# Performance work log

Measured on AMD Instinct MI355X. Metric: run time of the kernel, lower is better.

The kernel has to match this reference:

```python
import jax, jax.numpy as jnp
import numpy as np

HIDDEN = 768
HEADS = 12
ORDERS = 3
NEG = -1e9


def setup_inputs() -> dict:
    key = jax.random.key(0)
    ks = jax.random.split(key, 16)
    B, N = 8, 512
    s = 0.02
    inp = {
        "v": jax.random.normal(ks[0], (B, N, HIDDEN), jnp.float32),
        "k": jax.random.normal(ks[1], (B, N, HIDDEN), jnp.float32),
        "q": jax.random.normal(ks[2], (B, N, HIDDEN), jnp.float32),
        "masks": jax.random.bernoulli(ks[3], 0.1, (ORDERS, B, 1, N, N)),
        "tau": 1,
        "training": 0,
        "Wv": jax.random.normal(ks[4], (HIDDEN, HIDDEN), jnp.float32) * s,
        "bv": jnp.zeros((HIDDEN,), jnp.float32),
        "Wk": jax.random.normal(ks[5], (HIDDEN, HIDDEN), jnp.float32) * s,
        "bk": jnp.zeros((HIDDEN,), jnp.float32),
        "Wq": jax.random.normal(ks[6], (HIDDEN, HIDDEN), jnp.float32) * s,
        "bq": jnp.zeros((HIDDEN,), jnp.float32),
        "Wm": jax.random.normal(ks[7], (HIDDEN, HIDDEN), jnp.float32) * s,
        "bm": jnp.zeros((HIDDEN,), jnp.float32),
        "pool_w": jax.random.normal(ks[8], (HIDDEN, 1), jnp.float32) * s,
        "pool_b": jnp.zeros((1,), jnp.float32),
        "mlp_w1": jax.random.normal(ks[9], (HIDDEN, HIDDEN // 2), jnp.float32) * s,
        "mlp_w2": jax.random.normal(ks[10], (HIDDEN // 2, ORDERS), jnp.float32) * s,
        "mlp_b2": jnp.zeros((ORDERS,), jnp.float32),
    }
    return inp


def _soft_routing(x, pool_w, pool_b, mlp_w1, mlp_w2, mlp_b2):
    # pooling='fc': masked attention pooling over sequence, then 2-layer MLP + softmax
    pad = (jnp.sum(jnp.abs(x), axis=-1) == 0)[:, :, None]        # [B, N, 1]
    scores = x @ pool_w + pool_b                                  # [B, N, 1]
    scores = jnp.where(pad, NEG, scores)
    scores = jax.nn.softmax(scores, axis=1)
    pooled = jnp.sum(x * scores, axis=1)                          # [B, HIDDEN]
    logits = jax.nn.relu(pooled @ mlp_w1) @ mlp_w2 + mlp_b2       # [B, L]
    return jax.nn.softmax(logits, axis=-1)


def reference(v, k, q, masks, tau, training, Wv, bv, Wk, bk, Wq, bq, Wm, bm,
              pool_w, pool_b, mlp_w1, mlp_w2, mlp_b2):
    B, N, _ = q.shape
    dk = HIDDEN // HEADS
    alphas = _soft_routing(v, pool_w, pool_b, mlp_w1, mlp_w2, mlp_b2)  # [B, L]

    def split_heads(x):
        return x.reshape(B, N, HEADS, dk).transpose(0, 2, 1, 3)  # [B, H, N, dk]

    vh = split_heads(v @ Wv + bv)
    kh = split_heads(k @ Wk + bk)
    qh = split_heads(q @ Wq + bq)

    scores = jnp.einsum('bhnd,bhmd->bhnm', qh, kh) / jnp.sqrt(jnp.float32(dk))
    # masks: [L, B, 1, N, N] broadcast over heads -> att_list [L, B, H, N, N]
    masked = jnp.where(masks[:, :, :, :, :], NEG, scores[None])
    att_list = jax.nn.softmax(masked, axis=-1)                    # [L, B, H, N, N]
    att_map = jnp.einsum('bl,lbhnm->bhnm', alphas, att_list)
    atted = jnp.einsum('bhnm,bhmd->bhnd', att_map, vh)
    atted = atted.transpose(0, 2, 1, 3).reshape(B, N, HIDDEN)
    return atted @ Wm + bm
```

## Files before the change

### kernel.cpp

```cpp
#include <hip/hip_runtime.h>
#include <hip/hip_bf16.h>
#include <stdint.h>


typedef __bf16 bf16x8 __attribute__((ext_vector_type(8)));
typedef float f32x4 __attribute__((ext_vector_type(4)));

#define NEGV -1e9f
#define SBFE(x, off) (((int)((x) << (31 - (off)))) >> 31)

__device__ __forceinline__ float b2f(unsigned short h) {
    union { unsigned int u; float f; } x; x.u = ((unsigned int)h) << 16; return x.f;
}
__device__ __forceinline__ unsigned short f2b(float f) {
    union { float f; unsigned int u; } x; x.f = f;
    unsigned int u = x.u + 0x7FFFu + ((x.u >> 16) & 1u);
    return (unsigned short)(u >> 16);
}
__device__ __forceinline__ unsigned int packbf(unsigned int u0, unsigned int u1) {
    unsigned int r0 = (u0 + 0x7FFFu + ((u0 >> 16) & 1u)) >> 16;
    unsigned int r1 = (u1 + 0x7FFFu + ((u1 >> 16) & 1u)) & 0xFFFF0000u;
    return r0 | r1;
}
__device__ __forceinline__ uint4 load8bf(const void* base, size_t elemOff, int isF32) {
    if (!isF32) return *(const uint4*)((const unsigned short*)base + elemOff);
    const uint4* f = (const uint4*)((const float*)base + elemOff);
    uint4 a = f[0], b = f[1];
    uint4 r;
    r.x = packbf(a.x, a.y);
    r.y = packbf(a.z, a.w);
    r.z = packbf(b.x, b.y);
    r.w = packbf(b.z, b.w);
    return r;
}
__device__ __forceinline__ float loadF(const void* p, int idx, int isF32) {
    return isF32 ? ((const float*)p)[idx] : b2f(((const unsigned short*)p)[idx]);
}

__global__ void sniff_kernel(const unsigned int* __restrict__ mp,
                             const unsigned int* __restrict__ vp,
                             const unsigned int* __restrict__ wp,
                             int* __restrict__ flags)
{
    __shared__ int oki, oku, okf, badv, badw;
    if (threadIdx.x == 0) { oki = 1; oku = 1; okf = 1; badv = 0; badw = 0; }
    __syncthreads();
    int li = 1, lu = 1, lf = 1, bv = 0, bw = 0;
    const uint4* m4 = (const uint4*)mp;
    for (int i = threadIdx.x; i < 4096; i += 256) {
        uint4 u = m4[i];
        unsigned int ws[4] = {u.x, u.y, u.z, u.w};
        #pragma unroll
        for (int j = 0; j < 4; j++) {
            unsigned int w = ws[j];
            if (w > 1u) li = 0;
            if (w & 0xFEFEFEFEu) lu = 0;
            if (w != 0u && w != 0x3F800000u) lf = 0;
        }
    }
    const uint4* v4 = (const uint4*)vp;
    const uint4* w4 = (const uint4*)wp;
    for (int i = threadIdx.x; i < 2048; i += 256) {
        uint4 u = v4[i];
        uint4 u2 = w4[i];
        unsigned int wa[4] = {u.x, u.y, u.z, u.w};
        unsigned int wb[4] = {u2.x, u2.y, u2.z, u2.w};
        #pragma unroll
        for (int j = 0; j < 4; j++) {
            float f0 = b2f((unsigned short)(wa[j] & 0xFFFF));
            float f1 = b2f((unsigned short)(wa[j] >> 16));
            if (!(fabsf(f0) < 1e4f) || !(fabsf(f1) < 1e4f)) bv = 1;
            f0 = b2f((unsigned short)(wb[j] & 0xFFFF));
            f1 = b2f((unsigned short)(wb[j] >> 16));
            if (!(fabsf(f0) < 1e4f) || !(fabsf(f1) < 1e4f)) bw = 1;
        }
    }
    if (!li) atomicAnd(&oki, 0);
    if (!lu) atomicAnd(&oku, 0);
    if (!lf) atomicAnd(&okf, 0);
    if (bv) atomicOr(&badv, 1);
    if (bw) atomicOr(&badw, 1);
    __syncthreads();
    if (threadIdx.x == 0) {
        flags[0] = oki ? 0 : (oku ? 1 : (okf ? 2 : 3));
        flags[1] = badv;
        flags[2] = badw;
    }
}

__global__ __launch_bounds__(256) void conv_act_kernel(
        const void* __restrict__ v, const void* __restrict__ k,
        const void* __restrict__ q, const int* __restrict__ flags,
        unsigned short* __restrict__ vb, unsigned short* __restrict__ kb,
        unsigned short* __restrict__ qb)
{
    const int dtV = flags[1];
    const int which = blockIdx.y;
    const void* src = (which == 0) ? v : (which == 1) ? k : q;
    unsigned short* dst = (which == 0) ? vb : (which == 1) ? kb : qb;
    size_t off = ((size_t)blockIdx.x * 256 + threadIdx.x) * 8;
    uint4 r = load8bf(src, off, dtV);
    *(uint4*)(dst + off) = r;
}

__global__ __launch_bounds__(256) void conv_wt_kernel(
        const void* __restrict__ W0, const void* __restrict__ W1,
        const void* __restrict__ W2, const void* __restrict__ W3,
        const int* __restrict__ flags,
        unsigned short* __restrict__ T0, unsigned short* __restrict__ T1,
        unsigned short* __restrict__ T2, unsigned short* __restrict__ T3)
{
    __shared__ unsigned short tile[64][65];
    const int t = threadIdx.x;
    const int dtW = flags[2];
    const int which = blockIdx.y;
    const void* W = (which == 0) ? W0 : (which == 1) ? W1 : (which == 2) ? W2 : W3;
    unsigned short* T = (which == 0) ? T0 : (which == 1) ? T1 : (which == 2) ? T2 : T3;
    const int tk = (blockIdx.x / 12) << 6;
    const int tn = (blockIdx.x % 12) << 6;
    #pragma unroll
    for (int i = 0; i < 16; i++) {
        int idx = (i << 8) + t;
        int r = idx >> 6, c = idx & 63;
        tile[r][c] = f2b(loadF(W, (tk + r) * 768 + tn + c, dtW));
    }
    __syncthreads();
    #pragma unroll
    for (int i = 0; i < 16; i++) {
        int idx = (i << 8) + t;
        int rn = idx >> 6, ck = idx & 63;
        T[(size_t)(tn + rn) * 768 + tk + ck] = tile[ck][rn];
    }
}

__global__ __launch_bounds__(256) void pack_kernel(
        const void* __restrict__ masks, const int* __restrict__ flags,
        unsigned int* __restrict__ pm)
{
    __shared__ unsigned char flg[32 * 512];
    const int t = threadIdx.x;
    const int mode = flags[0];
    const size_t e0 = (size_t)blockIdx.x * (32 * 512);
    if (mode == 0 || mode == 2) {
        const uint4* p = (const uint4*)((const unsigned int*)masks + e0);
        for (int i = t; i < 4096; i += 256) {
            uint4 u = p[i];
            int base = i << 2;
            flg[base + 0] = u.x ? 1 : 0;
            flg[base + 1] = u.y ? 1 : 0;
            flg[base + 2] = u.z ? 1 : 0;
            flg[base + 3] = u.w ? 1 : 0;
        }
    } else if (mode == 1) {
        const uint4* p = (const uint4*)((const unsigned char*)masks + e0);
        for (int i = t; i < 1024; i += 256) {
            uint4 u = p[i];
            unsigned int uu[4] = {u.x, u.y, u.z, u.w};
            int base = i << 4;
            #pragma unroll
            for (int k2 = 0; k2 < 4; k2++)
                #pragma unroll
                for (int bb = 0; bb < 4; bb++)
                    flg[base + k2 * 4 + bb] = ((uu[k2] >> (bb * 8)) & 0xFFu) ? 1 : 0;
        }
    } else {
        const uint4* p = (const uint4*)((const unsigned short*)masks + e0);
        for (int i = t; i < 2048; i += 256) {
            uint4 u = p[i];
            unsigned int uu[4] = {u.x, u.y, u.z, u.w};
            int base = i << 3;
            #pragma unroll
            for (int k2 = 0; k2 < 4; k2++) {
                flg[base + k2 * 2 + 0] = (uu[k2] & 0xFFFFu) ? 1 : 0;
                flg[base + k2 * 2 + 1] = (uu[k2] >> 16) ? 1 : 0;
            }
        }
    }
    __syncthreads();
    const int lbi = blockIdx.x >> 4;
    const int qb0 = (blockIdx.x & 15) << 1;
    for (int widx = t; widx < 512; widx += 256) {
        const int qq = widx >> 8, sub = widx & 255;
        const int w2 = sub >> 6, lm = (sub >> 2) & 15, quad = sub & 3;
        const unsigned char* fr = &flg[(((qq << 4) + (quad << 2)) << 9) + lm];
        unsigned int bits = 0;
        #pragma unroll
        for (int rg = 0; rg < 4; rg++)
            #pragma unroll
            for (int nt = 0; nt < 8; nt++)
                bits |= ((unsigned int)(fr[(rg << 9) + (((w2 << 3) + nt) << 4)] & 1u))
                        << ((rg << 3) + nt);
        pm[(size_t)lbi * 8192 + (size_t)(qb0 + qq) * 256 + sub] = bits;
    }
}

__global__ __launch_bounds__(256) void route_score_kernel(
        const void* __restrict__ v, const void* __restrict__ pool_w,
        const void* __restrict__ pool_b, const int* __restrict__ flags,
        float* __restrict__ scores)
{
    __shared__ float pw[768];
    const int t = threadIdx.x;
    const int b = blockIdx.x >> 3, ch = blockIdx.x & 7;
    const int dtV = flags[1], dtW = flags[2];
    for (int d = t; d < 768; d += 256) pw[d] = loadF(pool_w, d, dtW);
    __syncthreads();
    const int r = t >> 2, c4 = t & 3;
    const int n = (ch << 6) + r;
    float dot = 0.f, asum = 0.f;
    if (!dtV) {
        const unsigned int* vr = (const unsigned int*)v + ((size_t)(b * 512 + n)) * 384;
        for (int j = 0; j < 96; j++) {
            int p = c4 + (j << 2);
            unsigned int u = vr[p];
            float f0 = b2f((unsigned short)(u & 0xFFFF));
            float f1 = b2f((unsigned short)(u >> 16));
            asum += fabsf(f0) + fabsf(f1);
            dot += f0 * pw[2 * p] + f1 * pw[2 * p + 1];
        }
    } else {
        const float* vf = (const float*)v + ((size_t)(b * 512 + n)) * 768;
        for (int j = 0; j < 48; j++) {
            float4 u = ((const float4*)vf)[c4 + (j << 2)];
            int e = (c4 + (j << 2)) << 2;
            asum += fabsf(u.x) + fabsf(u.y) + fabsf(u.z) + fabsf(u.w);
            dot += u.x * pw[e] + u.y * pw[e + 1] + u.z * pw[e + 2] + u.w * pw[e + 3];
        }
    }
    dot += __shfl_xor(dot, 1); dot += __shfl_xor(dot, 2);
    asum += __shfl_xor(asum, 1); asum += __shfl_xor(asum, 2);
    if (c4 == 0)
        scores[b * 512 + n] = (asum == 0.f) ? NEGV : dot + loadF(pool_b, 0, dtW);
}

__global__ __launch_bounds__(512) void route_softmax_kernel(
        const float* __restrict__ scores, float* __restrict__ scs)
{
    __shared__ float red[8];
    const int t = threadIdx.x, b = blockIdx.x;
    float scv = scores[b * 512 + t];
    float mx = scv;
    #pragma unroll
    for (int off = 1; off < 64; off <<= 1) mx = fmaxf(mx, __shfl_xor(mx, off));
    if ((t & 63) == 0) red[t >> 6] = mx;
    __syncthreads();
    float M = red[0];
    #pragma unroll
    for (int i = 1; i < 8; i++) M = fmaxf(M, red[i]);
    float e = __expf(scv - M);
    __syncthreads();
    float sm = e;
    #pragma unroll
    for (int off = 1; off < 64; off <<= 1) sm += __shfl_xor(sm, off);
    if ((t & 63) == 0) red[t >> 6] = sm;
    __syncthreads();
    float SS = 0.f;
    #pragma unroll
    for (int i = 0; i < 8; i++) SS += red[i];
    scs[b * 512 + t] = e / SS;
}

__global__ __launch_bounds__(256) void route_pool_kernel(
        const void* __restrict__ v, const int* __restrict__ flags,
        const float* __restrict__ scs, float* __restrict__ ppart)
{
    __shared__ float ps[64];
    const int t = threadIdx.x;
    const int ch = blockIdx.x, b = blockIdx.y;
    const int dtV = flags[1];
    if (t < 64) ps[t] = scs[b * 512 + (ch << 6) + t];
    __syncthreads();
    const int d0 = t * 3;
    float a0 = 0.f, a1 = 0.f, a2 = 0.f;
    if (!dtV) {
        const unsigned short* vb = (const unsigned short*)v
            + ((size_t)(b * 512 + (ch << 6))) * 768 + d0;
        #pragma unroll 4
        for (int r = 0; r < 64; r++) {
            float p = ps[r];
            a0 += b2f(vb[0]) * p; a1 += b2f(vb[1]) * p; a2 += b2f(vb[2]) * p;
            vb += 768;
        }
    } else {
        const float* vb = (const float*)v + ((size_t)(b * 512 + (ch << 6))) * 768 + d0;
        #pragma unroll 4
        for (int r = 0; r < 64; r++) {
            float p = ps[r];
            a0 += vb[0] * p; a1 += vb[1] * p; a2 += vb[2] * p;
            vb += 768;
        }
    }
    float* o = ppart + ((size_t)(b * 8 + ch)) * 768 + d0;
    o[0] = a0; o[1] = a1; o[2] = a2;
}

__global__ __launch_bounds__(256) void route_hid_kernel(
        const void* __restrict__ w1, const void* __restrict__ w2,
        const int* __restrict__ flags, const float* __restrict__ ppart,
        float* __restrict__ plog)
{
    __shared__ float pool[768];
    __shared__ float red[4][32];
    const int t = threadIdx.x;
    const int jc = blockIdx.x, b = blockIdx.y;
    const int dtW = flags[2];
    for (int d = t; d < 768; d += 256) {
        float a = 0.f;
        #pragma unroll
        for (int c = 0; c < 8; c++) a += ppart[((size_t)(b * 8 + c)) * 768 + d];
        pool[d] = a;
    }
    __syncthreads();
    const int jo = (t & 3) << 3;
    const int dr = t >> 2;
    float acc[8];
    #pragma unroll
    for (int j = 0; j < 8; j++) acc[j] = 0.f;
    for (int it = 0; it < 12; it++) {
        int d = (it << 6) + dr;
        float pv = pool[d];
        size_t off = (size_t)d * 384 + (jc << 5) + jo;
        if (!dtW) {
            uint4 u = *(const uint4*)((const unsigned short*)w1 + off);
            unsigned int uu[4] = {u.x, u.y, u.z, u.w};
            #pragma unroll
            for (int j2 = 0; j2 < 4; j2++) {
                acc[2 * j2]     += pv * b2f((unsigned short)(uu[j2] & 0xFFFF));
                acc[2 * j2 + 1] += pv * b2f((unsigned short)(uu[j2] >> 16));
            }
        } else {
            const float4* f = (const float4*)((const float*)w1 + off);
            float4 u0 = f[0], u1 = f[1];
            acc[0] += pv * u0.x; acc[1] += pv * u0.y;
            acc[2] += pv * u0.z; acc[3] += pv * u0.w;
            acc[4] += pv * u1.x; acc[5] += pv * u1.y;
            acc[6] += pv * u1.z; acc[7] += pv * u1.w;
        }
    }
    #pragma unroll
    for (int off = 4; off < 64; off <<= 1)
        #pragma unroll
        for (int j = 0; j < 8; j++) acc[j] += __shfl_xor(acc[j], off);
    const int w = t >> 6, lane = t & 63;
    if (lane < 4) {
        #pragma unroll
        for (int j = 0; j < 8; j++) red[w][lane * 8 + j] = acc[j];
    }
    __syncthreads();
    if (t < 32) {
        float h = red[0][t] + red[1][t] + red[2][t] + red[3][t];
        h = fmaxf(h, 0.f);
        int jg = (jc << 5) + t;
        float l0 = h * loadF(w2, jg * 3 + 0, dtW);
        float l1 = h * loadF(w2, jg * 3 + 1, dtW);
        float l2 = h * loadF(w2, jg * 3 + 2, dtW);
        #pragma unroll
        for (int off = 1; off < 32; off <<= 1) {
            l0 += __shfl_xor(l0, off);
            l1 += __shfl_xor(l1, off);
            l2 += __shfl_xor(l2, off);
        }
        if (t == 0) {
            float* o = plog + ((size_t)(b * 12 + jc)) * 3;
            o[0] = l0; o[1] = l1; o[2] = l2;
        }
    }
}

__global__ __launch_bounds__(64) void route_alpha_kernel(
        const void* __restrict__ b2, const int* __restrict__ flags,
        const float* __restrict__ plog, float* __restrict__ alphas)
{
    const int t = threadIdx.x, b = blockIdx.x;
    if (t == 0) {
        const int dtW = flags[2];
        float lg[3];
        #pragma unroll
        for (int l = 0; l < 3; l++) {
            float a = loadF(b2, l, dtW);
            for (int jc = 0; jc < 12; jc++) a += plog[((size_t)(b * 12 + jc)) * 3 + l];
            lg[l] = a;
        }
        float mm = fmaxf(lg[0], fmaxf(lg[1], lg[2]));
        float e0 = __expf(lg[0] - mm), e1 = __expf(lg[1] - mm), e2 = __expf(lg[2] - mm);
        float ss = e0 + e1 + e2;
        alphas[b * 3 + 0] = e0 / ss;
        alphas[b * 3 + 1] = e1 / ss;
        alphas[b * 3 + 2] = e2 / ss;
    }
}

__global__ __launch_bounds__(256) void gemm3_kernel(
        const unsigned short* __restrict__ X0, const unsigned short* __restrict__ X1,
        const unsigned short* __restrict__ X2,
        const unsigned short* __restrict__ W0, const unsigned short* __restrict__ W1,
        const unsigned short* __restrict__ W2,
        const void* __restrict__ bias0, const void* __restrict__ bias1,
        const void* __restrict__ bias2,
        const int* __restrict__ flags,
        void* __restrict__ dst0, void* __restrict__ dst1, void* __restrict__ dst2,
        int m0, int m1, int m2)
{
    __shared__ unsigned short smem[8192];
    unsigned short* At = smem;
    unsigned short* Bt = smem + 4096;
    const int t = threadIdx.x;
    const int which = blockIdx.y;
    const unsigned short* X  = (which == 0) ? X0 : (which == 1) ? X1 : X2;
    const unsigned short* WT = (which == 0) ? W0 : (which == 1) ? W1 : W2;
    const void* bias = (which == 0) ? bias0 : (which == 1) ? bias1 : bias2;
    void* dst = (which == 0) ? dst0 : (which == 1) ? dst1 : dst2;
    const int mode = (which == 0) ? m0 : (which == 1) ? m1 : m2;

    const int id = blockIdx.x;
    const int bx = id >> 6, by = id & 63;
    const int row0 = by << 6, col0 = bx << 6;
    const int w = t >> 6, lane = t & 63, quad = lane >> 4, lm = lane & 15;
    const int r0 = t >> 3, c0 = (t & 7) << 3;
    const int wr0 = r0 * 64 + (c0 ^ ((r0 & 7) << 3));
    const int dtW = flags[2];
    const int dtOut = flags[1];

    const unsigned short* xp  = X  + (size_t)(row0 + r0) * 768 + c0;
    const unsigned short* xp2 = xp + 32 * 768;
    const unsigned short* wp  = WT + (size_t)(col0 + r0) * 768 + c0;
    const unsigned short* wp2 = wp + 32 * 768;

    uint4 a0 = *(const uint4*)xp,  a1 = *(const uint4*)xp2;
    uint4 g0 = *(const uint4*)wp,  g1 = *(const uint4*)wp2;

    f32x4 acc[4];
    #pragma unroll
    for (int i = 0; i < 4; i++) acc[i] = (f32x4){0.f, 0.f, 0.f, 0.f};

    const int am = (w << 4) + lm;
    const int abase = am * 64, akey = (am & 7) << 3;

    for (int k0 = 0;;) {
        __syncthreads();
        *(uint4*)&At[wr0] = a0;        *(uint4*)&At[wr0 + 2048] = a1;
        *(uint4*)&Bt[wr0] = g0;        *(uint4*)&Bt[wr0 + 2048] = g1;
        __syncthreads();
        k0 += 64;
        if (k0 < 768) {
            a0 = *(const uint4*)(xp + k0);  a1 = *(const uint4*)(xp2 + k0);
            g0 = *(const uint4*)(wp + k0);  g1 = *(const uint4*)(wp2 + k0);
        }
        #pragma unroll
        for (int ks = 0; ks < 2; ks++) {
            int ko = (quad << 3) + (ks << 5);
            bf16x8 afr = *(const bf16x8*)&At[abase + (ko ^ akey)];
            #pragma unroll
            for (int t4 = 0; t4 < 4; t4++) {
                int bn = (t4 << 4) + lm;
                bf16x8 bfr = *(const bf16x8*)&Bt[bn * 64 + (ko ^ ((bn & 7) << 3))];
                acc[t4] = __builtin_amdgcn_mfma_f32_16x16x32_bf16(afr, bfr, acc[t4], 0, 0, 0);
            }
        }
        if (k0 >= 768) break;
    }

    if (mode == 1 && dtOut) {
        #pragma unroll
        for (int t4 = 0; t4 < 4; t4++) {
            int col = col0 + (t4 << 4) + lm;
            float bsv = loadF(bias, col, dtW);
            #pragma unroll
            for (int rg = 0; rg < 4; rg++) {
                int row = row0 + (w << 4) + (quad << 2) + rg;
                ((float*)dst)[(size_t)row * 768 + col] = acc[t4][rg] + bsv;
            }
        }
        return;
    }

    __syncthreads();
    #pragma unroll
    for (int t4 = 0; t4 < 4; t4++) {
        int colL = (t4 << 4) + lm;
        float bsv = loadF(bias, col0 + colL, dtW);
        #pragma unroll
        for (int rg = 0; rg < 4; rg++) {
            int rowL = (w << 4) + (quad << 2) + rg;
            unsigned short hv = f2b(acc[t4][rg] + bsv);
            if (mode == 2) smem[colL * 72 + rowL] = hv;
            else           smem[rowL * 72 + colL] = hv;
        }
    }
    __syncthreads();
    const int g = t >> 2, cc = (t & 3) << 4;
    uint4 o0 = *(const uint4*)&smem[g * 72 + cc];
    uint4 o1 = *(const uint4*)&smem[g * 72 + cc + 8];
    unsigned short* o;
    if (mode == 0) {
        int b = row0 >> 9, n0b = row0 & 511, h = col0 >> 6;
        o = (unsigned short*)dst + ((size_t)(b * 12 + h) * 512 + n0b + g) * 64 + cc;
    } else if (mode == 2) {
        int b = row0 >> 9, n0b = row0 & 511, h = col0 >> 6;
        o = (unsigned short*)dst + ((size_t)(b * 12 + h) * 64 + g) * 512 + n0b + cc;
    } else {
        o = (unsigned short*)dst + (size_t)(row0 + g) * 768 + col0 + cc;
    }
    *(uint4*)o = o0;
    *(uint4*)(o + 8) = o1;
}

__global__ __launch_bounds__(256) void attn_kernel(
        const unsigned short* __restrict__ qh, const unsigned short* __restrict__ kh,
        const unsigned short* __restrict__ vT, const unsigned int* __restrict__ pm,
        const float* __restrict__ alphas, unsigned short* __restrict__ atted)
{
    __shared__ unsigned short P[32 * 512];
    __shared__ float Zp[4][32][3];
    __shared__ unsigned short Ost[32 * 72];
    const int t = threadIdx.x;
    const int w = t >> 6, lane = t & 63, quad = lane >> 4, lm = lane & 15;
    const int id = blockIdx.x;
    const int bh = id % 96, qb2 = id / 96;
    const int b = bh / 12, h = bh % 12;
    const int n0 = qb2 << 5;

    const unsigned int* pmb = pm + (size_t)b * 8192 + (size_t)(qb2 << 1) * 256
                                 + (w << 6) + (lm << 2) + quad;
    unsigned int mw[2][3];
    #pragma unroll
    for (int s = 0; s < 2; s++) {
        mw[s][0] = pmb[s * 256];
        mw[s][1] = pmb[s * 256 + 65536];
        mw[s][2] = pmb[s * 256 + 131072];
    }

    float al[3];
    #pragma unroll
    for (int l = 0; l < 3; l++) al[l] = alphas[b * 3 + l];

    bf16x8 qa[2][2];
    #pragma unroll
    for (int s = 0; s < 2; s++) {
        const unsigned short* qrow = qh + ((size_t)(bh * 512 + n0 + (s << 4) + lm)) * 64
                                        + (quad << 3);
        qa[s][0] = *(const bf16x8*)qrow;
        qa[s][1] = *(const bf16x8*)(qrow + 32);
    }

    f32x4 acc[2][8];
    #pragma unroll
    for (int s = 0; s < 2; s++)
        #pragma unroll
        for (int i = 0; i < 8; i++) acc[s][i] = (f32x4){0.f, 0.f, 0.f, 0.f};

    const unsigned short* kb0 = kh + ((size_t)(bh * 512 + (w << 7) + lm)) * 64 + (quad << 3);
    __builtin_amdgcn_s_setprio(1);
    #pragma unroll
    for (int nt = 0; nt < 8; nt++) {
        const unsigned short* kr = kb0 + nt * (16 * 64);
        bf16x8 k0 = *(const bf16x8*)kr;
        bf16x8 k1 = *(const bf16x8*)(kr + 32);
        acc[0][nt] = __builtin_amdgcn_mfma_f32_16x16x32_bf16(qa[0][0], k0, acc[0][nt], 0, 0, 0);
        acc[1][nt] = __builtin_amdgcn_mfma_f32_16x16x32_bf16(qa[1][0], k0, acc[1][nt], 0, 0, 0);
        acc[0][nt] = __builtin_amdgcn_mfma_f32_16x16x32_bf16(qa[0][1], k1, acc[0][nt], 0, 0, 0);
        acc[1][nt] = __builtin_amdgcn_mfma_f32_16x16x32_bf16(qa[1][1], k1, acc[1][nt], 0, 0, 0);
    }
    __builtin_amdgcn_s_setprio(0);

    #pragma unroll
    for (int s = 0; s < 2; s++)
        #pragma unroll
        for (int nt = 0; nt < 8; nt++)
            #pragma unroll
            for (int rg = 0; rg < 4; rg++)
                acc[s][nt][rg] = __expf(acc[s][nt][rg] * 0.125f);

    unsigned int im[2][3];
    #pragma unroll
    for (int s = 0; s < 2; s++)
        #pragma unroll
        for (int l = 0; l < 3; l++) im[s][l] = ~mw[s][l];

    #pragma unroll
    for (int s = 0; s < 2; s++) {
        #pragma unroll
        for (int rg = 0; rg < 4; rg++) {
            float z0 = 0.f, z1 = 0.f, z2 = 0.f;
            #pragma unroll
            for (int nt = 0; nt < 8; nt++) {
                const int bp = (rg << 3) + nt;
                const unsigned int e = __float_as_uint(acc[s][nt][rg]);
                z0 += __uint_as_float(e & (unsigned int)SBFE(im[s][0], bp));
                z1 += __uint_as_float(e & (unsigned int)SBFE(im[s][1], bp));
                z2 += __uint_as_float(e & (unsigned int)SBFE(im[s][2], bp));
            }
            #pragma unroll
            for (int off = 1; off < 16; off <<= 1) {
                z0 += __shfl_xor(z0, off);
                z1 += __shfl_xor(z1, off);
                z2 += __shfl_xor(z2, off);
            }
            if (lm == 0) {
                int row = (s << 4) + (quad << 2) + rg;
                Zp[w][row][0] = z0; Zp[w][row][1] = z1; Zp[w][row][2] = z2;
            }
        }
    }
    __syncthreads();

    #pragma unroll
    for (int s = 0; s < 2; s++) {
        #pragma unroll
        for (int rg = 0; rg < 4; rg++) {
            const int row = (quad << 2) + rg;
            const int prow = (s << 4) + row;
            float addu = 0.f;
            unsigned int cb[3];
            #pragma unroll
            for (int l = 0; l < 3; l++) {
                float Z = Zp[0][prow][l] + Zp[1][prow][l] + Zp[2][prow][l] + Zp[3][prow][l];
                float c;
                if (Z > 0.f) c = al[l] * __builtin_amdgcn_rcpf(Z);
                else { c = 0.f; addu += al[l] * (1.0f / 512.0f); }
                cb[l] = __float_as_uint(c);
            }
            const int key = row & 7;
            const int pbase = prow * 512 + (lm & 7) + (w << 7)
                            + ((((lm >> 3) ^ key) & 1) << 3);
            const int kk16 = (key >> 1) << 4;
            #pragma unroll
            for (int nt = 0; nt < 8; nt++) {
                const int bp = (rg << 3) + nt;
                float wsum = __uint_as_float(cb[0] & (unsigned int)SBFE(im[s][0], bp))
                           + __uint_as_float(cb[1] & (unsigned int)SBFE(im[s][1], bp))
                           + __uint_as_float(cb[2] & (unsigned int)SBFE(im[s][2], bp));
                float p = fmaf(acc[s][nt][rg], wsum, addu);
                unsigned int u = __float_as_uint(p) + 0x8000u;
                P[pbase + ((nt << 4) ^ kk16)] = (unsigned short)(u >> 16);
            }
        }
    }

    const unsigned short* vb = vT + ((size_t)(bh * 64 + (w << 4) + lm)) * 512 + (quad << 3);
    bf16x8 vp0 = *(const bf16x8*)vb;
    bf16x8 vp1 = *(const bf16x8*)(vb + 32);
    __syncthreads();

    f32x4 accO0 = (f32x4){0.f, 0.f, 0.f, 0.f};
    f32x4 accO1 = (f32x4){0.f, 0.f, 0.f, 0.f};
    __builtin_amdgcn_s_setprio(1);
    #pragma unroll
    for (int ks = 0; ks < 16; ks++) {
        const int po = ((((ks << 2) + quad) ^ (lm & 7)) << 3);
        bf16x8 pa0 = *(const bf16x8*)&P[lm * 512 + po];
        bf16x8 pa1 = *(const bf16x8*)&P[(lm + 16) * 512 + po];
        bf16x8 vf = (ks == 0) ? vp0 : (ks == 1) ? vp1 : *(const bf16x8*)(vb + (ks << 5));
        accO0 = __builtin_amdgcn_mfma_f32_16x16x32_bf16(pa0, vf, accO0, 0, 0, 0);
        accO1 = __builtin_amdgcn_mfma_f32_16x16x32_bf16(pa1, vf, accO1, 0, 0, 0);
    }
    __builtin_amdgcn_s_setprio(0);
    #pragma unroll
    for (int rg = 0; rg < 4; rg++) {
        unsigned int u0 = __float_as_uint(accO0[rg]) + 0x8000u;
        unsigned int u1 = __float_as_uint(accO1[rg]) + 0x8000u;
        Ost[((quad << 2) + rg) * 72 + (w << 4) + lm] = (unsigned short)(u0 >> 16);
        Ost[(16 + (quad << 2) + rg) * 72 + (w << 4) + lm] = (unsigned short)(u1 >> 16);
    }
    __syncthreads();
    const int r2 = t >> 4, c4 = t & 15;
    #pragma unroll
    for (int rr = 0; rr < 2; rr++) {
        const int row = (rr << 4) + r2;
        uint2 val = *(const uint2*)&Ost[row * 72 + (c4 << 2)];
        *(uint2*)&atted[((size_t)(b * 512 + n0 + row)) * 768 + (h << 6) + (c4 << 2)] = val;
    }
}

extern "C" void kernel_launch(void* const* d_in, const int* in_sizes, int n_in,
                              void* d_out, int out_size, void* d_ws, size_t ws_size,
                              hipStream_t stream)
{
    const void* v  = d_in[0];
    const void* k  = d_in[1];
    const void* q  = d_in[2];
    const void* mk = d_in[3];
    const void* Wv = d_in[6];
    const void* bv = d_in[7];
    const void* Wk = d_in[8];
    const void* bk = d_in[9];
    const void* Wq = d_in[10];
    const void* bq = d_in[11];
    const void* Wm = d_in[12];
    const void* bm = d_in[13];
    const void* pool_w = d_in[14];
    const void* pool_b = d_in[15];
    const void* w1 = d_in[16];
    const void* w2 = d_in[17];
    const void* b2 = d_in[18];

    char* ws = (char*)d_ws;
    int*   flags  = (int*)ws;
    float* alphas = (float*)(ws + 256);
    float* scores = (float*)(ws + 512);
    float* scs    = (float*)(ws + 16896);
    float* ppart  = (float*)(ws + 33280);
    float* plog   = (float*)(ws + 229888);
    unsigned int* pm = (unsigned int*)(ws + 262144);
    unsigned short* qh  = (unsigned short*)(ws + 1048576);
    unsigned short* kh  = (unsigned short*)(ws + 1048576 + 1 * 6291456L);
    unsigned short* vT  = (unsigned short*)(ws + 1048576 + 2 * 6291456L);
    unsigned short* vb  = (unsigned short*)(ws + 1048576 + 3 * 6291456L);
    unsigned short* kb  = (unsigned short*)(ws + 1048576 + 4 * 6291456L);
    unsigned short* qb  = (unsigned short*)(ws + 1048576 + 5 * 6291456L);
    unsigned short* atted = vb;
    char* wt0 = ws + 1048576 + 6 * 6291456L;
    unsigned short* WTv = (unsigned short*)(wt0);
    unsigned short* WTk = (unsigned short*)(wt0 + 1 * 1179648L);
    unsigned short* WTq = (unsigned short*)(wt0 + 2 * 1179648L);
    unsigned short* WTm = (unsigned short*)(wt0 + 3 * 1179648L);

    sniff_kernel<<<dim3(1), dim3(256), 0, stream>>>(
        (const unsigned int*)mk, (const unsigned int*)v, (const unsigned int*)Wv, flags);
    conv_act_kernel<<<dim3(1536, 3), dim3(256), 0, stream>>>(v, k, q, flags, vb, kb, qb);
    conv_wt_kernel<<<dim3(144, 4), dim3(256), 0, stream>>>(
        Wv, Wk, Wq, Wm, flags, WTv, WTk, WTq, WTm);
    pack_kernel<<<dim3(384), dim3(256), 0, stream>>>(mk, flags, pm);
    route_score_kernel<<<dim3(64), dim3(256), 0, stream>>>(v, pool_w, pool_b, flags, scores);
    route_softmax_kernel<<<dim3(8), dim3(512), 0, stream>>>(scores, scs);
    route_pool_kernel<<<dim3(8, 8), dim3(256), 0, stream>>>(v, flags, scs, ppart);
    route_hid_kernel<<<dim3(12, 8), dim3(256), 0, stream>>>(w1, w2, flags, ppart, plog);
    route_alpha_kernel<<<dim3(8), dim3(64), 0, stream>>>(b2, flags, plog, alphas);
    gemm3_kernel<<<dim3(768, 3), dim3(256), 0, stream>>>(
        vb, kb, qb, WTv, WTk, WTq, bv, bk, bq, flags,
        (void*)vT, (void*)kh, (void*)qh, 2, 0, 0);
    attn_kernel<<<dim3(1536), dim3(256), 0, stream>>>(qh, kh, vT, pm, alphas, atted);
    gemm3_kernel<<<dim3(768, 1), dim3(256), 0, stream>>>(
        atted, atted, atted, WTm, WTm, WTm, bm, bm, bm, flags,
        d_out, d_out, d_out, 1, 1, 1);
}
```

Measured before the change: 273.5 us.

## Enlarge GEMM tiles to 128x128 with direct global-to-LDS loads

The projection GEMM kernel moves from 64x64 output tiles with one 16-row strip per wave to 128x128 tiles where each wave computes a 64x64 sub-tile (4x4 MFMA accumulators). Operands are staged with global_load_lds, which writes straight into shared memory using an XOR swizzle instead of going through registers. The register-prefetch double buffering is dropped in favour of load-then-sync per k-step. The aim is more operand reuse per LDS read and fewer blocks, at the cost of more registers, fewer blocks (192 per matrix), and exposed load latency.

```diff
diff --git a/kernel.cpp b/kernel.cpp
--- a/kernel.cpp
+++ b/kernel.cpp
@@ -35,6 +35,12 @@
 }
 __device__ __forceinline__ float loadF(const void* p, int idx, int isF32) {
     return isF32 ? ((const float*)p)[idx] : b2f(((const unsigned short*)p)[idx]);
+}
+__device__ __forceinline__ void gload16(const unsigned short* g, unsigned short* l) {
+    __builtin_amdgcn_global_load_lds(
+        (__attribute__((address_space(1))) void*)g,
+        (__attribute__((address_space(3))) void*)l,
+        16, 0, 0);
 }
 
 __global__ void sniff_kernel(const unsigned int* __restrict__ mp,
@@ -401,9 +407,9 @@
         void* __restrict__ dst0, void* __restrict__ dst1, void* __restrict__ dst2,
         int m0, int m1, int m2)
 {
-    __shared__ unsigned short smem[8192];
+    __shared__ unsigned short smem[17408];
     unsigned short* At = smem;
-    unsigned short* Bt = smem + 4096;
+    unsigned short* Bt = smem + 8192;
     const int t = threadIdx.x;
     const int which = blockIdx.y;
     const unsigned short* X  = (which == 0) ? X0 : (which == 1) ? X1 : X2;
@@ -413,96 +419,113 @@
     const int mode = (which == 0) ? m0 : (which == 1) ? m1 : m2;
 
     const int id = blockIdx.x;
-    const int bx = id >> 6, by = id & 63;
-    const int row0 = by << 6, col0 = bx << 6;
+    const int by = id & 31, bx = id >> 5;
+    const int row0 = by << 7, col0 = bx << 7;
     const int w = t >> 6, lane = t & 63, quad = lane >> 4, lm = lane & 15;
-    const int r0 = t >> 3, c0 = (t & 7) << 3;
-    const int wr0 = r0 * 64 + (c0 ^ ((r0 & 7) << 3));
+    const int wr = w >> 1, wc = w & 1;
     const int dtW = flags[2];
     const int dtOut = flags[1];
 
-    const unsigned short* xp  = X  + (size_t)(row0 + r0) * 768 + c0;
-    const unsigned short* xp2 = xp + 32 * 768;
-    const unsigned short* wp  = WT + (size_t)(col0 + r0) * 768 + c0;
-    const unsigned short* wp2 = wp + 32 * 768;
-
-    uint4 a0 = *(const uint4*)xp,  a1 = *(const uint4*)xp2;
-    uint4 g0 = *(const uint4*)wp,  g1 = *(const uint4*)wp2;
-
-    f32x4 acc[4];
-    #pragma unroll
-    for (int i = 0; i < 4; i++) acc[i] = (f32x4){0.f, 0.f, 0.f, 0.f};
-
-    const int am = (w << 4) + lm;
-    const int abase = am * 64, akey = (am & 7) << 3;
-
-    for (int k0 = 0;;) {
+    const int lr = lane >> 3;
+    const int lc8 = (((lane & 7) ^ lr) << 3);
+    const unsigned short* ga = X  + (size_t)(row0 + (w << 5) + lr) * 768 + lc8;
+    const unsigned short* gb = WT + (size_t)(col0 + (w << 5) + lr) * 768 + lc8;
+    unsigned short* la = At + (w << 11);
+    unsigned short* lb = Bt + (w << 11);
+
+    const int arow = (wr << 6) + lm;
+    const int brow = (wc << 6) + lm;
+    const int koff[2] = { ((quad ^ (lm & 7)) << 3), (((4 + quad) ^ (lm & 7)) << 3) };
+
+    f32x4 acc[4][4];
+    #pragma unroll
+    for (int m = 0; m < 4; m++)
+        #pragma unroll
+        for (int n = 0; n < 4; n++) acc[m][n] = (f32x4){0.f, 0.f, 0.f, 0.f};
+
+    for (int k0 = 0; k0 < 768; k0 += 64) {
+        if (k0) __syncthreads();
+        #pragma unroll
+        for (int i = 0; i < 4; i++) {
+            gload16(ga + (i << 3) * 768 + k0, la + (i << 9));
+            gload16(gb + (i << 3) * 768 + k0, lb + (i << 9));
+        }
         __syncthreads();
-        *(uint4*)&At[wr0] = a0;        *(uint4*)&At[wr0 + 2048] = a1;
-        *(uint4*)&Bt[wr0] = g0;        *(uint4*)&Bt[wr0 + 2048] = g1;
-        __syncthreads();
-        k0 += 64;
-        if (k0 < 768) {
-            a0 = *(const uint4*)(xp + k0);  a1 = *(const uint4*)(xp2 + k0);
-            g0 = *(const uint4*)(wp + k0);  g1 = *(const uint4*)(wp2 + k0);
-        }
         #pragma unroll
         for (int ks = 0; ks < 2; ks++) {
-            int ko = (quad << 3) + (ks << 5);
-            bf16x8 afr = *(const bf16x8*)&At[abase + (ko ^ akey)];
-            #pragma unroll
-            for (int t4 = 0; t4 < 4; t4++) {
-                int bn = (t4 << 4) + lm;
-                bf16x8 bfr = *(const bf16x8*)&Bt[bn * 64 + (ko ^ ((bn & 7) << 3))];
-                acc[t4] = __builtin_amdgcn_mfma_f32_16x16x32_bf16(afr, bfr, acc[t4], 0, 0, 0);
-            }
-        }
-        if (k0 >= 768) break;
+            const int ko = koff[ks];
+            bf16x8 af[4], bfr[4];
+            #pragma unroll
+            for (int m = 0; m < 4; m++)
+                af[m] = *(const bf16x8*)&At[(arow + (m << 4)) * 64 + ko];
+            #pragma unroll
+            for (int n = 0; n < 4; n++)
+                bfr[n] = *(const bf16x8*)&Bt[(brow + (n << 4)) * 64 + ko];
+            #pragma unroll
+            for (int m = 0; m < 4; m++)
+                #pragma unroll
+                for (int n = 0; n < 4; n++)
+                    acc[m][n] = __builtin_amdgcn_mfma_f32_16x16x32_bf16(
+                        af[m], bfr[n], acc[m][n], 0, 0, 0);
+        }
     }
 
     if (mode == 1 && dtOut) {
         #pragma unroll
-        for (int t4 = 0; t4 < 4; t4++) {
-            int col = col0 + (t4 << 4) + lm;
+        for (int n = 0; n < 4; n++) {
+            int col = col0 + (wc << 6) + (n << 4) + lm;
             float bsv = loadF(bias, col, dtW);
             #pragma unroll
+            for (int m = 0; m < 4; m++)
+                #pragma unroll
+                for (int rg = 0; rg < 4; rg++) {
+                    int row = row0 + (wr << 6) + (m << 4) + (quad << 2) + rg;
+                    ((float*)dst)[(size_t)row * 768 + col] = acc[m][n][rg] + bsv;
+                }
+        }
+        return;
+    }
+
+    __syncthreads();
+    #pragma unroll
+    for (int n = 0; n < 4; n++) {
+        int colL = (wc << 6) + (n << 4) + lm;
+        float bsv = loadF(bias, col0 + colL, dtW);
+        #pragma unroll
+        for (int m = 0; m < 4; m++)
+            #pragma unroll
             for (int rg = 0; rg < 4; rg++) {
-                int row = row0 + (w << 4) + (quad << 2) + rg;
-                ((float*)dst)[(size_t)row * 768 + col] = acc[t4][rg] + bsv;
-            }
-        }
-        return;
-    }
-
-    __syncthreads();
-    #pragma unroll
-    for (int t4 = 0; t4 < 4; t4++) {
-        int colL = (t4 << 4) + lm;
-        float bsv = loadF(bias, col0 + colL, dtW);
-        #pragma unroll
-        for (int rg = 0; rg < 4; rg++) {
-            int rowL = (w << 4) + (quad << 2) + rg;
-            unsigned short hv = f2b(acc[t4][rg] + bsv);
-            if (mode == 2) smem[colL * 72 + rowL] = hv;
-            else           smem[rowL * 72 + colL] = hv;
-        }
-    }
-    __syncthreads();
-    const int g = t >> 2, cc = (t & 3) << 4;
-    uint4 o0 = *(const uint4*)&smem[g * 72 + cc];
-    uint4 o1 = *(const uint4*)&smem[g * 72 + cc + 8];
-    unsigned short* o;
-    if (mode == 0) {
-        int b = row0 >> 9, n0b = row0 & 511, h = col0 >> 6;
-        o = (unsigned short*)dst + ((size_t)(b * 12 + h) * 512 + n0b + g) * 64 + cc;
-    } else if (mode == 2) {
-        int b = row0 >> 9, n0b = row0 & 511, h = col0 >> 6;
-        o = (unsigned short*)dst + ((size_t)(b * 12 + h) * 64 + g) * 512 + n0b + cc;
-    } else {
-        o = (unsigned short*)dst + (size_t)(row0 + g) * 768 + col0 + cc;
-    }
-    *(uint4*)o = o0;
-    *(uint4*)(o + 8) = o1;
+                int rowL = (wr << 6) + (m << 4) + (quad << 2) + rg;
+                unsigned short hv = f2b(acc[m][n][rg] + bsv);
+                if (mode == 2) smem[colL * 136 + rowL] = hv;
+                else           smem[rowL * 136 + colL] = hv;
+            }
+    }
+    __syncthreads();
+    const int g = t >> 2, ccq = (t & 3) << 5;
+    const int b = row0 >> 9, n0b = row0 & 511, h0 = col0 >> 6;
+    #pragma unroll
+    for (int rr = 0; rr < 2; rr++) {
+        const int r = g + (rr << 6);
+        #pragma unroll
+        for (int hf = 0; hf < 2; hf++) {
+            const int cc = ccq + (hf << 4);
+            uint4 o0 = *(const uint4*)&smem[r * 136 + cc];
+            uint4 o1 = *(const uint4*)&smem[r * 136 + cc + 8];
+            unsigned short* o;
+            if (mode == 0) {
+                int h = h0 + (cc >> 6), d = cc & 63;
+                o = (unsigned short*)dst + ((size_t)(b * 12 + h) * 512 + n0b + r) * 64 + d;
+            } else if (mode == 2) {
+                int h = h0 + (r >> 6), d = r & 63;
+                o = (unsigned short*)dst + ((size_t)(b * 12 + h) * 64 + d) * 512 + n0b + cc;
+            } else {
+                o = (unsigned short*)dst + (size_t)(row0 + r) * 768 + col0 + cc;
+            }
+            *(uint4*)o = o0;
+            *(uint4*)(o + 8) = o1;
+        }
+    }
 }
 
 __global__ __launch_bounds__(256) void attn_kernel(
@@ -726,11 +749,11 @@
     route_pool_kernel<<<dim3(8, 8), dim3(256), 0, stream>>>(v, flags, scs, ppart);
     route_hid_kernel<<<dim3(12, 8), dim3(256), 0, stream>>>(w1, w2, flags, ppart, plog);
     route_alpha_kernel<<<dim3(8), dim3(64), 0, stream>>>(b2, flags, plog, alphas);
-    gemm3_kernel<<<dim3(768, 3), dim3(256), 0, stream>>>(
+    gemm3_kernel<<<dim3(192, 3), dim3(256), 0, stream>>>(
         vb, kb, qb, WTv, WTk, WTq, bv, bk, bq, flags,
         (void*)vT, (void*)kh, (void*)qh, 2, 0, 0);
     attn_kernel<<<dim3(1536), dim3(256), 0, stream>>>(qh, kh, vT, pm, alphas, atted);
-    gemm3_kernel<<<dim3(768, 1), dim3(256), 0, stream>>>(
+    gemm3_kernel<<<dim3(192, 1), dim3(256), 0, stream>>>(
         atted, atted, atted, WTm, WTm, WTm, bm, bm, bm, flags,
         d_out, d_out, d_out, 1, 1, 1);
 }
```

New measurement: 281.6 us. 3.0% more time.
